# Kernel tuning notes

Hardware: AMD Instinct MI355X
Metric: run time of the kernel (lower is better)

The kernel has to match this reference:

```python
import jax, jax.numpy as jnp
import numpy as np

RES = 1024
NUM_ROOMS = 8
N_AGENTS = 5_000_000


def setup_inputs() -> dict:
    key = jax.random.key(0)
    k1, k2, k3 = jax.random.split(key, 3)
    agent_positions = jax.random.uniform(k1, (N_AGENTS, 2), dtype=jnp.float32)
    room_params = jax.random.uniform(k2, (NUM_ROOMS, 4), dtype=jnp.float32)
    # torch init: params[:, 2:] = params[:, 2:] * 0.1 + 0.05  (room sigmas)
    room_params = room_params.at[:, 2:].set(room_params[:, 2:] * 0.1 + 0.05)
    wall_density = jax.random.uniform(k3, (RES, RES), dtype=jnp.float32)
    return {
        "agent_positions": agent_positions,
        "room_params": room_params,
        "wall_density": wall_density,
    }


def reference(agent_positions, room_params, wall_density):
    res = wall_density.shape[0]
    lin = jnp.linspace(0.0, 1.0, res, dtype=wall_density.dtype)
    x_grid, y_grid = jnp.meshgrid(lin, lin, indexing="ij")  # [res,res]

    # Per-room Gaussian density maps, vectorized over rooms -> [R,res,res]
    cx = room_params[:, 0, None, None]
    cy = room_params[:, 1, None, None]
    sx = room_params[:, 2, None, None]
    sy = room_params[:, 3, None, None]
    spatial_layout = jnp.exp(
        -((x_grid - cx) ** 2 / (2.0 * sx**2) + (y_grid - cy) ** 2 / (2.0 * sy**2))
    )

    # Agent flow histogram via single fused scatter-add
    ix = jnp.clip((agent_positions[:, 0] * res).astype(jnp.int32), 0, res - 1)
    iy = jnp.clip((agent_positions[:, 1] * res).astype(jnp.int32), 0, res - 1)
    flow_field = jnp.zeros((res, res), dtype=wall_density.dtype).at[ix, iy].add(1.0)
    flow_field = flow_field / (flow_field.max() + 1e-6)

    dynamic_layout = spatial_layout * (1.0 - wall_density[None, :, :])
    return (dynamic_layout, flow_field)
```

## Files before the change

### kernel.cpp

```cpp
#include <hip/hip_runtime.h>

#define RES 1024
#define NROOMS 8
#define NBUCKETS 256
#define BINS_PER_BUCKET (4 * RES)
#define CAP 32768
#define SWPB 8
#define F4PT 8
#define AGB 8192

__global__ __launch_bounds__(512) void scatter_kernel(
    const float4* __restrict__ pos, int n4, int nagents,
    unsigned short* __restrict__ buf, unsigned int* __restrict__ cursor)
{
    __shared__ unsigned int   cnt[SWPB][NBUCKETS];
    __shared__ unsigned int   sbase[SWPB][NBUCKETS];
    __shared__ unsigned int   pstart[NBUCKETS];
    __shared__ unsigned int   ptotal[NBUCKETS];
    __shared__ unsigned int   gbase[NBUCKETS];
    __shared__ unsigned int   wsum[4];
    __shared__ unsigned short staged[AGB];

    int tid  = threadIdx.x;
    int wv   = tid >> 6;
    int lane = tid & 63;

    #pragma unroll
    for (int i = 0; i < (SWPB * NBUCKETS) / 512; ++i)
        ((unsigned int*)cnt)[tid + 512 * i] = 0u;
    __syncthreads();

    unsigned int   code[2 * F4PT];
    unsigned short rank[2 * F4PT];
    int base4 = blockIdx.x * (AGB / 2);
    #pragma unroll
    for (int k = 0; k < F4PT; ++k) {
        int i4 = base4 + (k << 9) + tid;
        if (i4 < n4) {
            float4 p = pos[i4];
            int ix0 = min(max((int)(p.x * 1024.0f), 0), 1023);
            int iy0 = min(max((int)(p.y * 1024.0f), 0), 1023);
            int ix1 = min(max((int)(p.z * 1024.0f), 0), 1023);
            int iy1 = min(max((int)(p.w * 1024.0f), 0), 1023);
            unsigned int b0 = (unsigned int)(ix0 >> 2);
            unsigned int b1 = (unsigned int)(ix1 >> 2);
            code[2 * k]     = (b0 << 16) | (unsigned int)(((ix0 & 3) << 10) | iy0);
            code[2 * k + 1] = (b1 << 16) | (unsigned int)(((ix1 & 3) << 10) | iy1);
            rank[2 * k]     = (unsigned short)atomicAdd(&cnt[wv][b0], 1u);
            rank[2 * k + 1] = (unsigned short)atomicAdd(&cnt[wv][b1], 1u);
        } else {
            code[2 * k] = 0xFFFFFFFFu;
            code[2 * k + 1] = 0xFFFFFFFFu;
        }
    }
    __syncthreads();

    unsigned int run = 0;
    if (tid < NBUCKETS) {
        #pragma unroll
        for (int w = 0; w < SWPB; ++w) {
            unsigned int c = cnt[w][tid];
            sbase[w][tid] = run;
            run += c;
        }
        ptotal[tid] = run;
        gbase[tid]  = run ? atomicAdd(&cursor[tid], run) : 0u;
        unsigned int t = run;
        #pragma unroll
        for (int off = 1; off < 64; off <<= 1) {
            unsigned int v = (unsigned int)__shfl_up((int)t, off, 64);
            if (lane >= off) t += v;
        }
        if (lane == 63) wsum[wv] = t;
        pstart[tid] = t - run;
    }
    __syncthreads();
    if (tid < NBUCKETS) {
        unsigned int off = 0;
        #pragma unroll
        for (int w = 0; w < 3; ++w) if (w < wv) off += wsum[w];
        unsigned int ps = pstart[tid] + off;
        pstart[tid] = ps;
        #pragma unroll
        for (int w = 0; w < SWPB; ++w) sbase[w][tid] += ps;
    }
    __syncthreads();

    #pragma unroll
    for (int k = 0; k < 2 * F4PT; ++k) {
        unsigned int cd = code[k];
        if (cd != 0xFFFFFFFFu) {
            unsigned int b = cd >> 16;
            staged[sbase[wv][b] + rank[k]] = (unsigned short)(cd & 0xFFFFu);
        }
    }
    __syncthreads();

    #pragma unroll 4
    for (int bb = 0; bb < 32; ++bb) {
        int b = (wv << 5) + bb;
        unsigned int n  = ptotal[b];
        unsigned int ps = pstart[b];
        unsigned int gb = gbase[b];
        for (unsigned int e = lane; e < n; e += 64) {
            unsigned int p = gb + e;
            if (p < CAP) buf[b * CAP + p] = staged[ps + e];
        }
    }

    if (blockIdx.x == 0 && tid == 0 && (nagents & 1)) {
        const float* t = (const float*)pos;
        float px = t[2 * (nagents - 1)];
        float py = t[2 * (nagents - 1) + 1];
        int ix = min(max((int)(px * 1024.0f), 0), 1023);
        int iy = min(max((int)(py * 1024.0f), 0), 1023);
        unsigned int b = (unsigned int)(ix >> 2);
        unsigned int p = atomicAdd(&cursor[b], 1u);
        if (p < CAP) buf[b * CAP + p] = (unsigned short)(((ix & 3) << 10) | iy);
    }
}

__global__ __launch_bounds__(1024) void hist_build_kernel(
    const unsigned short* __restrict__ buf,
    const unsigned int* __restrict__ cursor,
    unsigned int* __restrict__ counts,
    unsigned int* __restrict__ out_max)
{
    __shared__ __align__(16) unsigned int h[BINS_PER_BUCKET];
    int b = blockIdx.x, tid = threadIdx.x;
    #pragma unroll
    for (int i = 0; i < BINS_PER_BUCKET / 1024; ++i) h[tid + 1024 * i] = 0u;
    __syncthreads();

    unsigned int n = min(cursor[b], (unsigned int)CAP);
    const unsigned short* seg = buf + (size_t)b * CAP;
    unsigned int n2 = n & ~1u;
    for (unsigned int i = 2 * tid; i < n2; i += 2048) {
        unsigned int u = *(const unsigned int*)(seg + i);
        atomicAdd(&h[u & 0xFFFFu], 1u);
        atomicAdd(&h[u >> 16], 1u);
    }
    if (tid == 0 && (n & 1)) atomicAdd(&h[seg[n - 1]], 1u);
    __syncthreads();

    uint4 v = ((const uint4*)h)[tid];
    ((uint4*)counts)[(size_t)b * (BINS_PER_BUCKET / 4) + tid] = v;
    unsigned int m = max(max(v.x, v.y), max(v.z, v.w));
    #pragma unroll
    for (int off = 32; off > 0; off >>= 1)
        m = max(m, (unsigned int)__shfl_down((int)m, off, 64));
    __shared__ unsigned int sm[16];
    if ((tid & 63) == 0) sm[tid >> 6] = m;
    __syncthreads();
    if (tid == 0) {
        #pragma unroll
        for (int w = 1; w < 16; ++w) m = max(m, sm[w]);
        atomicMax(out_max, m);
    }
}

__global__ __launch_bounds__(256) void hist_atomic_kernel(
    const float4* __restrict__ pos, int n4, int nagents,
    unsigned int* __restrict__ counts)
{
    int idx = blockIdx.x * blockDim.x + threadIdx.x;
    int stride = gridDim.x * blockDim.x;
    for (int i = idx; i < n4; i += stride) {
        float4 p = pos[i];
        int ix0 = min(max((int)(p.x * 1024.0f), 0), 1023);
        int iy0 = min(max((int)(p.y * 1024.0f), 0), 1023);
        int ix1 = min(max((int)(p.z * 1024.0f), 0), 1023);
        int iy1 = min(max((int)(p.w * 1024.0f), 0), 1023);
        atomicAdd(&counts[(ix0 << 10) + iy0], 1u);
        atomicAdd(&counts[(ix1 << 10) + iy1], 1u);
    }
    if (idx == 0 && (nagents & 1)) {
        const float* t = (const float*)pos;
        int ix = min(max((int)(t[2 * (nagents - 1)] * 1024.0f), 0), 1023);
        int iy = min(max((int)(t[2 * (nagents - 1) + 1] * 1024.0f), 0), 1023);
        atomicAdd(&counts[(ix << 10) + iy], 1u);
    }
}

__global__ __launch_bounds__(256) void max_kernel(
    const uint4* __restrict__ counts, unsigned int* __restrict__ out_max)
{
    int idx = blockIdx.x * blockDim.x + threadIdx.x;
    int stride = gridDim.x * blockDim.x;
    unsigned int m = 0;
    const int n4 = (RES * RES) / 4;
    for (int i = idx; i < n4; i += stride) {
        uint4 c = counts[i];
        m = max(m, max(max(c.x, c.y), max(c.z, c.w)));
    }
    #pragma unroll
    for (int off = 32; off > 0; off >>= 1)
        m = max(m, (unsigned int)__shfl_down((int)m, off, 64));
    __shared__ unsigned int sm[4];
    if ((threadIdx.x & 63) == 0) sm[threadIdx.x >> 6] = m;
    __syncthreads();
    if (threadIdx.x == 0) {
        m = max(max(sm[0], sm[1]), max(sm[2], sm[3]));
        atomicMax(out_max, m);
    }
}

__global__ __launch_bounds__(256) void final_kernel(
    const float* __restrict__ room_params,
    const float4* __restrict__ wall,
    float4* __restrict__ dyn,
    float* __restrict__ flow,
    const unsigned int* __restrict__ maxp)
{
    int idx = blockIdx.x * blockDim.x + threadIdx.x;
    int i  = idx >> 8;
    int j0 = (idx & 255) << 2;

    const float inv1023 = 1.0f / 1023.0f;
    float x  = (float)i * inv1023;
    float y0 = (float)(j0 + 0) * inv1023;
    float y1 = (float)(j0 + 1) * inv1023;
    float y2 = (float)(j0 + 2) * inv1023;
    float y3 = (float)(j0 + 3) * inv1023;

    float4 w = wall[idx];
    float omx = 1.0f - w.x;
    float omy = 1.0f - w.y;
    float omz = 1.0f - w.z;
    float omw = 1.0f - w.w;

    uint4 c = ((const uint4*)flow)[idx];
    float inv = 1.0f / ((float)(*maxp) + 1e-6f);
    ((float4*)flow)[idx] = make_float4((float)c.x * inv, (float)c.y * inv,
                                       (float)c.z * inv, (float)c.w * inv);

    const int plane4 = (RES * RES) / 4;
    #pragma unroll
    for (int r = 0; r < NROOMS; ++r) {
        float cx = room_params[4 * r + 0];
        float cy = room_params[4 * r + 1];
        float sx = room_params[4 * r + 2];
        float sy = room_params[4 * r + 3];
        float isx = 1.0f / (2.0f * sx * sx);
        float isy = 1.0f / (2.0f * sy * sy);
        float dx = x - cx;
        float ax = dx * dx * isx;
        float d0 = y0 - cy, d1 = y1 - cy, d2 = y2 - cy, d3 = y3 - cy;
        float4 d;
        d.x = __expf(-(ax + d0 * d0 * isy)) * omx;
        d.y = __expf(-(ax + d1 * d1 * isy)) * omy;
        d.z = __expf(-(ax + d2 * d2 * isy)) * omz;
        d.w = __expf(-(ax + d3 * d3 * isy)) * omw;
        dyn[(size_t)r * plane4 + idx] = d;
    }
}

extern "C" void kernel_launch(void* const* d_in, const int* in_sizes, int n_in,
                              void* d_out, int out_size, void* d_ws, size_t ws_size,
                              hipStream_t stream) {
    const float* agents      = (const float*)d_in[0];
    const float* room_params = (const float*)d_in[1];
    const float* wall        = (const float*)d_in[2];

    float* dyn  = (float*)d_out;
    float* flow = (float*)d_out + (size_t)NROOMS * RES * RES;
    unsigned int* counts = (unsigned int*)flow;

    int nagents = in_sizes[0] / 2;
    int n4 = nagents / 2;

    size_t need = 2048 + (size_t)NBUCKETS * CAP * sizeof(unsigned short);

    if (ws_size >= need) {
        unsigned int*   cursor = (unsigned int*)d_ws;
        unsigned int*   maxp   = (unsigned int*)((char*)d_ws + 1024);
        unsigned short* buf    = (unsigned short*)((char*)d_ws + 2048);

        hipMemsetAsync(d_ws, 0, 2048, stream);
        int nblk = (n4 + (AGB / 2) - 1) / (AGB / 2);
        scatter_kernel<<<nblk, 512, 0, stream>>>((const float4*)agents, n4, nagents,
                                                 buf, cursor);
        hist_build_kernel<<<NBUCKETS, 1024, 0, stream>>>(buf, cursor, counts, maxp);
        final_kernel<<<(RES * RES / 4) / 256, 256, 0, stream>>>(
            room_params, (const float4*)wall, (float4*)dyn, flow, maxp);
    } else {
        unsigned int* maxp = (unsigned int*)d_ws;
        hipMemsetAsync(flow, 0, (size_t)RES * RES * sizeof(float), stream);
        hipMemsetAsync(maxp, 0, sizeof(unsigned int), stream);
        hist_atomic_kernel<<<1280, 256, 0, stream>>>((const float4*)agents, n4, nagents, counts);
        max_kernel<<<256, 256, 0, stream>>>((const uint4*)counts, maxp);
        final_kernel<<<(RES * RES / 4) / 256, 256, 0, stream>>>(
            room_params, (const float4*)wall, (float4*)dyn, flow, maxp);
    }
}
```

Before: 124.1 us.

## Pack scatter registers, pair buffer writes, and use nontemporal loads/stores

The scatter kernel packs bucket, entry and rank into one 32-bit word with a validity bitmask. This cuts register use so a min-blocks launch bound of 6 can raise occupancy. The bucket write-out now skips empty buckets and writes aligned pairs of 16-bit entries as 32-bit stores. The final kernel and the agent reads use nontemporal loads and stores so streaming data bypasses the cache. These are several unrelated micro-optimizations, and the nontemporal flow reload could cost extra latency.

```diff
diff --git a/kernel.cpp b/kernel.cpp
--- a/kernel.cpp
+++ b/kernel.cpp
@@ -6,11 +6,13 @@
 #define BINS_PER_BUCKET (4 * RES)
 #define CAP 32768
 #define SWPB 8
-#define F4PT 8
 #define AGB 8192
 
-__global__ __launch_bounds__(512) void scatter_kernel(
-    const float4* __restrict__ pos, int n4, int nagents,
+typedef float  f32x4 __attribute__((ext_vector_type(4)));
+typedef unsigned int u32x4 __attribute__((ext_vector_type(4)));
+
+__global__ __launch_bounds__(512, 6) void scatter_kernel(
+    const f32x4* __restrict__ pos, int n4, int nagents,
     unsigned short* __restrict__ buf, unsigned int* __restrict__ cursor)
 {
     __shared__ unsigned int   cnt[SWPB][NBUCKETS];
@@ -30,33 +32,33 @@
         ((unsigned int*)cnt)[tid + 512 * i] = 0u;
     __syncthreads();
 
-    unsigned int   code[2 * F4PT];
-    unsigned short rank[2 * F4PT];
+    unsigned int pk[16];
+    unsigned int valid = 0u;
     int base4 = blockIdx.x * (AGB / 2);
     #pragma unroll
-    for (int k = 0; k < F4PT; ++k) {
+    for (int k = 0; k < 8; ++k) {
         int i4 = base4 + (k << 9) + tid;
         if (i4 < n4) {
-            float4 p = pos[i4];
+            f32x4 p = __builtin_nontemporal_load(&pos[i4]);
             int ix0 = min(max((int)(p.x * 1024.0f), 0), 1023);
             int iy0 = min(max((int)(p.y * 1024.0f), 0), 1023);
             int ix1 = min(max((int)(p.z * 1024.0f), 0), 1023);
             int iy1 = min(max((int)(p.w * 1024.0f), 0), 1023);
             unsigned int b0 = (unsigned int)(ix0 >> 2);
             unsigned int b1 = (unsigned int)(ix1 >> 2);
-            code[2 * k]     = (b0 << 16) | (unsigned int)(((ix0 & 3) << 10) | iy0);
-            code[2 * k + 1] = (b1 << 16) | (unsigned int)(((ix1 & 3) << 10) | iy1);
-            rank[2 * k]     = (unsigned short)atomicAdd(&cnt[wv][b0], 1u);
-            rank[2 * k + 1] = (unsigned short)atomicAdd(&cnt[wv][b1], 1u);
-        } else {
-            code[2 * k] = 0xFFFFFFFFu;
-            code[2 * k + 1] = 0xFFFFFFFFu;
-        }
-    }
-    __syncthreads();
-
-    unsigned int run = 0;
+            unsigned int e0 = (unsigned int)(((ix0 & 3) << 10) | iy0);
+            unsigned int e1 = (unsigned int)(((ix1 & 3) << 10) | iy1);
+            unsigned int r0 = atomicAdd(&cnt[wv][b0], 1u);
+            unsigned int r1 = atomicAdd(&cnt[wv][b1], 1u);
+            pk[2 * k]     = (b0 << 24) | (e0 << 12) | (r0 & 0xFFFu);
+            pk[2 * k + 1] = (b1 << 24) | (e1 << 12) | (r1 & 0xFFFu);
+            valid |= 3u << (2 * k);
+        }
+    }
+    __syncthreads();
+
     if (tid < NBUCKETS) {
+        unsigned int run = 0;
         #pragma unroll
         for (int w = 0; w < SWPB; ++w) {
             unsigned int c = cnt[w][tid];
@@ -87,24 +89,42 @@
     __syncthreads();
 
     #pragma unroll
-    for (int k = 0; k < 2 * F4PT; ++k) {
-        unsigned int cd = code[k];
-        if (cd != 0xFFFFFFFFu) {
-            unsigned int b = cd >> 16;
-            staged[sbase[wv][b] + rank[k]] = (unsigned short)(cd & 0xFFFFu);
-        }
-    }
-    __syncthreads();
-
-    #pragma unroll 4
+    for (int k = 0; k < 16; ++k) {
+        if (valid & (1u << k)) {
+            unsigned int cd = pk[k];
+            unsigned int b = cd >> 24;
+            staged[sbase[wv][b] + (cd & 0xFFFu)] =
+                (unsigned short)((cd >> 12) & 0xFFFu);
+        }
+    }
+    __syncthreads();
+
     for (int bb = 0; bb < 32; ++bb) {
         int b = (wv << 5) + bb;
-        unsigned int n  = ptotal[b];
+        unsigned int n = ptotal[b];
+        if (n == 0) continue;
         unsigned int ps = pstart[b];
         unsigned int gb = gbase[b];
-        for (unsigned int e = lane; e < n; e += 64) {
+        unsigned int head = gb & 1u;
+        if (head && lane == 0) {
+            if (gb < CAP) buf[b * CAP + gb] = staged[ps];
+        }
+        unsigned int body  = n - head;
+        unsigned int npair = body >> 1;
+        for (unsigned int q = lane; q < npair; q += 64) {
+            unsigned int e  = head + 2 * q;
+            unsigned int lo = staged[ps + e];
+            unsigned int hi = staged[ps + e + 1];
+            unsigned int p  = gb + e;
+            if (p + 1 < CAP)
+                *(unsigned int*)(buf + (size_t)b * CAP + p) = lo | (hi << 16);
+            else if (p < CAP)
+                buf[(size_t)b * CAP + p] = (unsigned short)lo;
+        }
+        if ((body & 1u) && lane == 0) {
+            unsigned int e = head + 2 * npair;
             unsigned int p = gb + e;
-            if (p < CAP) buf[b * CAP + p] = staged[ps + e];
+            if (p < CAP) buf[(size_t)b * CAP + p] = staged[ps + e];
         }
     }
 
@@ -143,8 +163,8 @@
     if (tid == 0 && (n & 1)) atomicAdd(&h[seg[n - 1]], 1u);
     __syncthreads();
 
-    uint4 v = ((const uint4*)h)[tid];
-    ((uint4*)counts)[(size_t)b * (BINS_PER_BUCKET / 4) + tid] = v;
+    u32x4 v = ((const u32x4*)h)[tid];
+    ((u32x4*)counts)[(size_t)b * (BINS_PER_BUCKET / 4) + tid] = v;
     unsigned int m = max(max(v.x, v.y), max(v.z, v.w));
     #pragma unroll
     for (int off = 32; off > 0; off >>= 1)
@@ -207,8 +227,8 @@
 
 __global__ __launch_bounds__(256) void final_kernel(
     const float* __restrict__ room_params,
-    const float4* __restrict__ wall,
-    float4* __restrict__ dyn,
+    const f32x4* __restrict__ wall,
+    f32x4* __restrict__ dyn,
     float* __restrict__ flow,
     const unsigned int* __restrict__ maxp)
 {
@@ -223,16 +243,20 @@
     float y2 = (float)(j0 + 2) * inv1023;
     float y3 = (float)(j0 + 3) * inv1023;
 
-    float4 w = wall[idx];
+    f32x4 w = __builtin_nontemporal_load(&wall[idx]);
     float omx = 1.0f - w.x;
     float omy = 1.0f - w.y;
     float omz = 1.0f - w.z;
     float omw = 1.0f - w.w;
 
-    uint4 c = ((const uint4*)flow)[idx];
+    u32x4 c = __builtin_nontemporal_load(&((const u32x4*)flow)[idx]);
     float inv = 1.0f / ((float)(*maxp) + 1e-6f);
-    ((float4*)flow)[idx] = make_float4((float)c.x * inv, (float)c.y * inv,
-                                       (float)c.z * inv, (float)c.w * inv);
+    f32x4 f;
+    f.x = (float)c.x * inv;
+    f.y = (float)c.y * inv;
+    f.z = (float)c.z * inv;
+    f.w = (float)c.w * inv;
+    __builtin_nontemporal_store(f, &((f32x4*)flow)[idx]);
 
     const int plane4 = (RES * RES) / 4;
     #pragma unroll
@@ -246,12 +270,12 @@
         float dx = x - cx;
         float ax = dx * dx * isx;
         float d0 = y0 - cy, d1 = y1 - cy, d2 = y2 - cy, d3 = y3 - cy;
-        float4 d;
+        f32x4 d;
         d.x = __expf(-(ax + d0 * d0 * isy)) * omx;
         d.y = __expf(-(ax + d1 * d1 * isy)) * omy;
         d.z = __expf(-(ax + d2 * d2 * isy)) * omz;
         d.w = __expf(-(ax + d3 * d3 * isy)) * omw;
-        dyn[(size_t)r * plane4 + idx] = d;
+        __builtin_nontemporal_store(d, &dyn[(size_t)r * plane4 + idx]);
     }
 }
 
@@ -276,20 +300,20 @@
         unsigned int*   maxp   = (unsigned int*)((char*)d_ws + 1024);
         unsigned short* buf    = (unsigned short*)((char*)d_ws + 2048);
 
-        hipMemsetAsync(d_ws, 0, 2048, stream);
+        (void)hipMemsetAsync(d_ws, 0, 2048, stream);
         int nblk = (n4 + (AGB / 2) - 1) / (AGB / 2);
-        scatter_kernel<<<nblk, 512, 0, stream>>>((const float4*)agents, n4, nagents,
+        scatter_kernel<<<nblk, 512, 0, stream>>>((const f32x4*)agents, n4, nagents,
                                                  buf, cursor);
         hist_build_kernel<<<NBUCKETS, 1024, 0, stream>>>(buf, cursor, counts, maxp);
         final_kernel<<<(RES * RES / 4) / 256, 256, 0, stream>>>(
-            room_params, (const float4*)wall, (float4*)dyn, flow, maxp);
+            room_params, (const f32x4*)wall, (f32x4*)dyn, flow, maxp);
     } else {
         unsigned int* maxp = (unsigned int*)d_ws;
-        hipMemsetAsync(flow, 0, (size_t)RES * RES * sizeof(float), stream);
-        hipMemsetAsync(maxp, 0, sizeof(unsigned int), stream);
+        (void)hipMemsetAsync(flow, 0, (size_t)RES * RES * sizeof(float), stream);
+        (void)hipMemsetAsync(maxp, 0, sizeof(unsigned int), stream);
         hist_atomic_kernel<<<1280, 256, 0, stream>>>((const float4*)agents, n4, nagents, counts);
         max_kernel<<<256, 256, 0, stream>>>((const uint4*)counts, maxp);
         final_kernel<<<(RES * RES / 4) / 256, 256, 0, stream>>>(
-            room_params, (const float4*)wall, (float4*)dyn, flow, maxp);
-    }
-}
+            room_params, (const f32x4*)wall, (f32x4*)dyn, flow, maxp);
+    }
+}
```

Measured after the change: 135.6 us. 1.09x slower.
